# Kernel optimization log

Hardware: AMD Instinct MI355X
Metric: run time of the kernel (lower is better)

## Reference

```python
import jax, jax.numpy as jnp
import numpy as np

B, S, D, C, WD, I = 8, 14, 2048, 20, 300, 1024  # batch, imgSize, imgFeatureDim, classNum, wordFeatureDim, intermediaDim


def setup_inputs() -> dict:
    key = jax.random.key(0)
    ks = jax.random.split(key, 8)
    s = 0.02
    return {
        "imgFeaturemap": jax.random.normal(ks[0], (B, S, S, D), jnp.float32),
        "wordFeatures": jax.random.normal(ks[1], (C, WD), jnp.float32),
        "W1": jax.random.normal(ks[2], (I, D), jnp.float32) * s,   # fc1, no bias
        "W2": jax.random.normal(ks[3], (I, WD), jnp.float32) * s,  # fc2, no bias
        "W3": jax.random.normal(ks[4], (I, I), jnp.float32) * s,   # fc3
        "b3": jax.random.normal(ks[5], (I,), jnp.float32) * s,
        "W4": jax.random.normal(ks[6], (1, I), jnp.float32) * s,   # fc4
        "b4": jax.random.normal(ks[7], (1,), jnp.float32) * s,
    }


def reference(imgFeaturemap, wordFeatures, W1, W2, W3, b3, W4, b4):
    b, s, _, d = imgFeaturemap.shape
    c = wordFeatures.shape[0]
    n = b * s * s  # number of spatial locations across batch

    h_img = imgFeaturemap.reshape(n, d) @ W1.T          # [N, I]
    h_word = wordFeatures @ W2.T                         # [C, I]
    # broadcasted elementwise product + tanh (original materializes via repeat)
    t = jnp.tanh(h_img[:, None, :] * h_word[None, :, :])  # [N, C, I]
    feat = t @ W3.T + b3                                  # [N, C, I]
    coef = (feat @ W4.T)[..., 0] + b4[0]                  # [N, C]
    # softmax over spatial positions per (batch, class)
    coef = jax.nn.softmax(coef.reshape(b, s * s, c), axis=1).reshape(b, s, s, c)
    # weighted feature map and class-wise pooled semantic features
    fmwc = imgFeaturemap[:, :, :, None, :] * coef[..., None]  # [B, S, S, C, D]
    semanticFeature = fmwc.sum(axis=(1, 2))                    # [B, C, D]
    return semanticFeature, fmwc, coef
```

## Files before the change

kernel.cpp:

```cpp
#include <hip/hip_runtime.h>

typedef __attribute__((ext_vector_type(4))) float float4_t;
typedef __attribute__((ext_vector_type(8))) short short8_t;
typedef __attribute__((ext_vector_type(4))) unsigned short ushort4_t;

#define B_ 8
#define S_ 14
#define P_ 196
#define N_ 1568
#define D_ 2048
#define C_ 20
#define WD_ 300
#define I_ 1024
#define PS_ 14

__device__ __forceinline__ unsigned short f2bf(float f) {
    unsigned u = __builtin_bit_cast(unsigned, f);
    u += 0x7FFFu + ((u >> 16) & 1u);
    return (unsigned short)(u >> 16);
}

__global__ __launch_bounds__(256) void cvt_prep_kernel(const float* __restrict__ img,
                                                       const float* __restrict__ W1,
                                                       unsigned short* __restrict__ Xb,
                                                       unsigned short* __restrict__ W1b,
                                                       const float* __restrict__ wf,
                                                       const float* __restrict__ W2,
                                                       const float* __restrict__ W3,
                                                       const float* __restrict__ b3,
                                                       const float* __restrict__ W4,
                                                       const float* __restrict__ b4,
                                                       float* __restrict__ hw,
                                                       float* __restrict__ we,
                                                       float* __restrict__ bias) {
    int bid = blockIdx.x, tid = threadIdx.x;
    if (bid < 5184) {
        const float* src;
        unsigned short* dst;
        int i4;
        if (bid < 3136) { i4 = bid * 256 + tid; src = img; dst = Xb; }
        else            { i4 = (bid - 3136) * 256 + tid; src = W1; dst = W1b; }
        float4_t v = ((const float4_t*)src)[i4];
        ushort4_t o;
        o.x = f2bf(v.x); o.y = f2bf(v.y); o.z = f2bf(v.z); o.w = f2bf(v.w);
        ((ushort4_t*)dst)[i4] = o;
        return;
    }
    int pb = bid - 5184;
    if (pb < 80) {
        int idx = pb * 256 + tid;
        int c = idx >> 10, i = idx & 1023;
        const float* wr  = wf + c * WD_;
        const float* w2r = W2 + i * WD_;
        float s = 0.f;
        #pragma unroll 4
        for (int k = 0; k < WD_; k++) s += wr[k] * w2r[k];
        hw[idx] = s;
    } else if (pb < 96) {
        __shared__ float red[256];
        int blk = pb - 80;
        int i0 = blk * 64;
        int q = tid >> 6, col = tid & 63;
        float s = 0.f;
        #pragma unroll 4
        for (int j = q * 256; j < q * 256 + 256; j++)
            s += W4[j] * W3[j * I_ + i0 + col];
        red[tid] = s;
        __syncthreads();
        if (tid < 64)
            we[i0 + tid] = red[tid] + red[tid + 64] + red[tid + 128] + red[tid + 192];
    } else {
        __shared__ float r[256];
        float s = 0.f;
        for (int j = tid; j < I_; j += 256) s += b3[j] * W4[j];
        r[tid] = s;
        __syncthreads();
        for (int o = 128; o > 0; o >>= 1) {
            if (tid < o) r[tid] += r[tid + o];
            __syncthreads();
        }
        if (tid == 0) bias[0] = r[0] + b4[0];
    }
}

__global__ __launch_bounds__(256) void gemm_himg_kernel(const unsigned short* __restrict__ Xb,
                                                        const unsigned short* __restrict__ W1b,
                                                        float* __restrict__ H) {
    int wave = blockIdx.x * 4 + (threadIdx.x >> 6);
    int lane = threadIdx.x & 63;
    int kjob = 0;
    if (wave >= 784) { kjob = 1; wave -= 784; }
    int mjob = wave >> 4;
    int njob = wave & 15;
    int m0 = mjob * 32, n0 = njob * 64;
    int ra = lane & 15;
    int kq = (lane >> 4) * 8;
    int kbase = kjob * 1024;

    float4_t acc[2][4] = {};
    const unsigned short* xa = Xb  + (size_t)(m0 + ra) * D_ + kbase + kq;
    const unsigned short* wb = W1b + (size_t)(n0 + ra) * D_ + kbase + kq;

    #pragma unroll 2
    for (int k0 = 0; k0 < 1024; k0 += 32) {
        short8_t a0 = *(const short8_t*)(xa + k0);
        short8_t a1 = *(const short8_t*)(xa + 16 * D_ + k0);
        short8_t b0 = *(const short8_t*)(wb + k0);
        short8_t b1 = *(const short8_t*)(wb + 16 * D_ + k0);
        short8_t b2 = *(const short8_t*)(wb + 32 * D_ + k0);
        short8_t b3v = *(const short8_t*)(wb + 48 * D_ + k0);
        acc[0][0] = __builtin_amdgcn_mfma_f32_16x16x32_bf16(a0, b0, acc[0][0], 0, 0, 0);
        acc[0][1] = __builtin_amdgcn_mfma_f32_16x16x32_bf16(a0, b1, acc[0][1], 0, 0, 0);
        acc[0][2] = __builtin_amdgcn_mfma_f32_16x16x32_bf16(a0, b2, acc[0][2], 0, 0, 0);
        acc[0][3] = __builtin_amdgcn_mfma_f32_16x16x32_bf16(a0, b3v, acc[0][3], 0, 0, 0);
        acc[1][0] = __builtin_amdgcn_mfma_f32_16x16x32_bf16(a1, b0, acc[1][0], 0, 0, 0);
        acc[1][1] = __builtin_amdgcn_mfma_f32_16x16x32_bf16(a1, b1, acc[1][1], 0, 0, 0);
        acc[1][2] = __builtin_amdgcn_mfma_f32_16x16x32_bf16(a1, b2, acc[1][2], 0, 0, 0);
        acc[1][3] = __builtin_amdgcn_mfma_f32_16x16x32_bf16(a1, b3v, acc[1][3], 0, 0, 0);
    }

    int col = lane & 15, rq = (lane >> 4) * 4;
    float* Hk = H + (size_t)kjob * N_ * I_;
    #pragma unroll
    for (int mt = 0; mt < 2; mt++) {
        #pragma unroll
        for (int nt = 0; nt < 4; nt++) {
            float4_t v = acc[mt][nt];
            int rbase = m0 + mt * 16 + rq;
            int cidx = n0 + nt * 16 + col;
            Hk[(rbase + 0) * I_ + cidx] = v.x;
            Hk[(rbase + 1) * I_ + cidx] = v.y;
            Hk[(rbase + 2) * I_ + cidx] = v.z;
            Hk[(rbase + 3) * I_ + cidx] = v.w;
        }
    }
}

__global__ __launch_bounds__(256) void logits_kernel(const float* __restrict__ H,
                                                     const float* __restrict__ hw,
                                                     const float* __restrict__ we,
                                                     const float* __restrict__ bias,
                                                     float* __restrict__ lg) {
    __shared__ float sh[4][I_];
    __shared__ float sw[I_];
    int n0 = blockIdx.x * 4, tid = threadIdx.x;
    #pragma unroll
    for (int t = 0; t < 4; t++) {
        int idx = tid + 256 * t;
        sw[idx] = we[idx];
        #pragma unroll
        for (int nn = 0; nn < 4; nn++)
            sh[nn][idx] = H[(size_t)(n0 + nn) * I_ + idx]
                        + H[(size_t)(N_ + n0 + nn) * I_ + idx];
    }
    __syncthreads();
    int wv = tid >> 6, lane = tid & 63;
    float bz = bias[0];
    for (int j = 0; j < 5; j++) {
        int c = j * 4 + wv;
        const float* hwc = hw + c * I_;
        float a0 = 0.f, a1 = 0.f, a2 = 0.f, a3 = 0.f;
        #pragma unroll 2
        for (int i = lane; i < I_; i += 64) {
            float hv = hwc[i], wvv = sw[i];
            float x0 = sh[0][i] * hv;
            float x1 = sh[1][i] * hv;
            float x2 = sh[2][i] * hv;
            float x3 = sh[3][i] * hv;
            float t0 = 1.f - __fdividef(2.f, __expf(2.f * x0) + 1.f);
            float t1 = 1.f - __fdividef(2.f, __expf(2.f * x1) + 1.f);
            float t2 = 1.f - __fdividef(2.f, __expf(2.f * x2) + 1.f);
            float t3 = 1.f - __fdividef(2.f, __expf(2.f * x3) + 1.f);
            a0 += t0 * wvv; a1 += t1 * wvv; a2 += t2 * wvv; a3 += t3 * wvv;
        }
        #pragma unroll
        for (int o = 32; o > 0; o >>= 1) {
            a0 += __shfl_down(a0, o);
            a1 += __shfl_down(a1, o);
            a2 += __shfl_down(a2, o);
            a3 += __shfl_down(a3, o);
        }
        if (lane == 0) {
            lg[(n0 + 0) * C_ + c] = a0 + bz;
            lg[(n0 + 1) * C_ + c] = a1 + bz;
            lg[(n0 + 2) * C_ + c] = a2 + bz;
            lg[(n0 + 3) * C_ + c] = a3 + bz;
        }
    }
}

__global__ __launch_bounds__(256) void softmax_kernel(const float* __restrict__ lg,
                                                      float* __restrict__ coef) {
    __shared__ float r[4];
    __shared__ float bval;
    int bx = blockIdx.x;
    int b = bx / C_, c = bx % C_;
    int tid = threadIdx.x, wv = tid >> 6, lane = tid & 63;
    float v = (tid < P_) ? lg[(b * P_ + tid) * C_ + c] : -3.0e38f;
    float m = v;
    #pragma unroll
    for (int o = 32; o > 0; o >>= 1) m = fmaxf(m, __shfl_down(m, o));
    if (lane == 0) r[wv] = m;
    __syncthreads();
    if (tid == 0) bval = fmaxf(fmaxf(r[0], r[1]), fmaxf(r[2], r[3]));
    __syncthreads();
    float mx = bval;
    float e = (tid < P_) ? __expf(v - mx) : 0.f;
    float s = e;
    #pragma unroll
    for (int o = 32; o > 0; o >>= 1) s += __shfl_down(s, o);
    __syncthreads();
    if (lane == 0) r[wv] = s;
    __syncthreads();
    if (tid == 0) bval = r[0] + r[1] + r[2] + r[3];
    __syncthreads();
    if (tid < P_) coef[(b * P_ + tid) * C_ + c] = e / bval;
}

__global__ __launch_bounds__(256) void fmwc_kernel(const float* __restrict__ img,
                                                   const float* __restrict__ coef,
                                                   float* __restrict__ fm) {
    __shared__ float sc[C_];
    int bp = blockIdx.x, tid = threadIdx.x;
    if (tid < C_) sc[tid] = coef[bp * C_ + tid];
    __syncthreads();
    const float4_t* ir = (const float4_t*)(img + (size_t)bp * D_);
    float4_t v0 = ir[tid], v1 = ir[tid + 256];
    float4_t* ob = (float4_t*)(fm + (size_t)bp * C_ * D_);
    #pragma unroll
    for (int c = 0; c < C_; c++) {
        float s = sc[c];
        ob[c * 512 + tid] = v0 * s;
        ob[c * 512 + tid + 256] = v1 * s;
    }
}

__global__ __launch_bounds__(256) void semantic_part_kernel(const float* __restrict__ img,
                                                            const float* __restrict__ coef,
                                                            float* __restrict__ part) {
    __shared__ float sc[PS_ * C_];
    int bx = blockIdx.x;
    int ps = bx >> 4;
    int b = (bx >> 1) & 7;
    int ch = bx & 1;
    int tid = threadIdx.x;
    for (int q = tid; q < PS_ * C_; q += 256)
        sc[q] = coef[(b * P_ + ps * PS_) * C_ + q];
    __syncthreads();
    const float4_t* base = (const float4_t*)(img + (size_t)(b * P_ + ps * PS_) * D_ + ch * 1024) + tid;
    float4_t acc[C_];
    #pragma unroll
    for (int c = 0; c < C_; c++) acc[c] = (float4_t){0.f, 0.f, 0.f, 0.f};
    for (int pp = 0; pp < PS_; pp++) {
        float4_t v = base[pp * 512];
        #pragma unroll
        for (int c = 0; c < C_; c++) acc[c] += v * sc[pp * C_ + c];
    }
    float* pb = part + ((size_t)(ps * B_ + b) * C_) * D_ + ch * 1024 + tid * 4;
    #pragma unroll
    for (int c = 0; c < C_; c++) *(float4_t*)(pb + c * D_) = acc[c];
}

__global__ __launch_bounds__(256) void semantic_reduce_kernel(const float* __restrict__ part,
                                                              float* __restrict__ sem) {
    int idx = blockIdx.x * 256 + threadIdx.x;
    const float4_t* p4 = (const float4_t*)part;
    float4_t s = {0.f, 0.f, 0.f, 0.f};
    #pragma unroll
    for (int ps = 0; ps < PS_; ps++) s += p4[(size_t)ps * 81920 + idx];
    ((float4_t*)sem)[idx] = s;
}

extern "C" void kernel_launch(void* const* d_in, const int* in_sizes, int n_in,
                              void* d_out, int out_size, void* d_ws, size_t ws_size,
                              hipStream_t stream) {
    const float* img = (const float*)d_in[0];
    const float* wf  = (const float*)d_in[1];
    const float* W1  = (const float*)d_in[2];
    const float* W2  = (const float*)d_in[3];
    const float* W3  = (const float*)d_in[4];
    const float* b3  = (const float*)d_in[5];
    const float* W4  = (const float*)d_in[6];
    const float* b4  = (const float*)d_in[7];

    float* out  = (float*)d_out;
    float* sem  = out;
    float* fm   = out + (size_t)B_ * C_ * D_;
    float* coef = fm + (size_t)N_ * C_ * D_;

    char* ws = (char*)d_ws;
    unsigned short* Xb  = (unsigned short*)ws;
    unsigned short* W1b = (unsigned short*)(ws + 6422528);
    float* H    = (float*)(ws + 10616832);
    float* hw   = (float*)(ws + 23461888);
    float* we   = (float*)(ws + 23543808);
    float* bias = (float*)(ws + 23547904);
    float* lg   = (float*)(ws + 23548160);
    float* part = (float*)(ws + 23673600);

    cvt_prep_kernel<<<5281, 256, 0, stream>>>(img, W1, Xb, W1b, wf, W2, W3, b3, W4, b4, hw, we, bias);
    gemm_himg_kernel<<<392, 256, 0, stream>>>(Xb, W1b, H);
    logits_kernel<<<N_ / 4, 256, 0, stream>>>(H, hw, we, bias, lg);
    softmax_kernel<<<B_ * C_, 256, 0, stream>>>(lg, coef);
    semantic_part_kernel<<<PS_ * B_ * 2, 256, 0, stream>>>(img, coef, part);
    semantic_reduce_kernel<<<320, 256, 0, stream>>>(part, sem);
    fmwc_kernel<<<N_, 256, 0, stream>>>(img, coef, fm);
}
```

Baseline: 427.6 us.

## Fuse image GEMM with logits computation, keeping H tile in shared memory

Merges the bf16 MFMA projection GEMM and the tanh/logit reduction into one kernel. Each 1024-thread block computes a 16-row tile of H, with two K-halves summed in LDS, then computes logits for those rows directly. This removes writing and rereading the full H intermediate and one launch, at the cost of far fewer blocks (98) and repeated reads of W1 per tile.

```diff
diff --git a/kernel.cpp b/kernel.cpp
--- a/kernel.cpp
+++ b/kernel.cpp
@@ -13,6 +13,7 @@
 #define WD_ 300
 #define I_ 1024
 #define PS_ 14
+#define HLD 1025
 
 __device__ __forceinline__ unsigned short f2bf(float f) {
     unsigned u = __builtin_bit_cast(unsigned, f);
@@ -83,109 +84,72 @@
     }
 }
 
-__global__ __launch_bounds__(256) void gemm_himg_kernel(const unsigned short* __restrict__ Xb,
-                                                        const unsigned short* __restrict__ W1b,
-                                                        float* __restrict__ H) {
-    int wave = blockIdx.x * 4 + (threadIdx.x >> 6);
-    int lane = threadIdx.x & 63;
-    int kjob = 0;
-    if (wave >= 784) { kjob = 1; wave -= 784; }
-    int mjob = wave >> 4;
-    int njob = wave & 15;
-    int m0 = mjob * 32, n0 = njob * 64;
-    int ra = lane & 15;
-    int kq = (lane >> 4) * 8;
+__global__ __launch_bounds__(1024) void gemm_logits_kernel(const unsigned short* __restrict__ Xb,
+                                                           const unsigned short* __restrict__ W1b,
+                                                           const float* __restrict__ hw,
+                                                           const float* __restrict__ we,
+                                                           const float* __restrict__ bias,
+                                                           float* __restrict__ lg) {
+    __shared__ float hsh[16 * HLD];
+    __shared__ float sw[I_];
+    int tid = threadIdx.x;
+    int wave = tid >> 6, lane = tid & 63;
+    int kjob = wave >> 3, nsl = wave & 7;
+    int n0 = nsl * 128;
+    int m0 = blockIdx.x * 16;
+    int ra = lane & 15, kq = (lane >> 4) * 8;
     int kbase = kjob * 1024;
-
-    float4_t acc[2][4] = {};
+    sw[tid] = we[tid];
+
     const unsigned short* xa = Xb  + (size_t)(m0 + ra) * D_ + kbase + kq;
     const unsigned short* wb = W1b + (size_t)(n0 + ra) * D_ + kbase + kq;
 
+    float4_t acc[8] = {};
     #pragma unroll 2
     for (int k0 = 0; k0 < 1024; k0 += 32) {
-        short8_t a0 = *(const short8_t*)(xa + k0);
-        short8_t a1 = *(const short8_t*)(xa + 16 * D_ + k0);
-        short8_t b0 = *(const short8_t*)(wb + k0);
-        short8_t b1 = *(const short8_t*)(wb + 16 * D_ + k0);
-        short8_t b2 = *(const short8_t*)(wb + 32 * D_ + k0);
-        short8_t b3v = *(const short8_t*)(wb + 48 * D_ + k0);
-        acc[0][0] = __builtin_amdgcn_mfma_f32_16x16x32_bf16(a0, b0, acc[0][0], 0, 0, 0);
-        acc[0][1] = __builtin_amdgcn_mfma_f32_16x16x32_bf16(a0, b1, acc[0][1], 0, 0, 0);
-        acc[0][2] = __builtin_amdgcn_mfma_f32_16x16x32_bf16(a0, b2, acc[0][2], 0, 0, 0);
-        acc[0][3] = __builtin_amdgcn_mfma_f32_16x16x32_bf16(a0, b3v, acc[0][3], 0, 0, 0);
-        acc[1][0] = __builtin_amdgcn_mfma_f32_16x16x32_bf16(a1, b0, acc[1][0], 0, 0, 0);
-        acc[1][1] = __builtin_amdgcn_mfma_f32_16x16x32_bf16(a1, b1, acc[1][1], 0, 0, 0);
-        acc[1][2] = __builtin_amdgcn_mfma_f32_16x16x32_bf16(a1, b2, acc[1][2], 0, 0, 0);
-        acc[1][3] = __builtin_amdgcn_mfma_f32_16x16x32_bf16(a1, b3v, acc[1][3], 0, 0, 0);
-    }
-
-    int col = lane & 15, rq = (lane >> 4) * 4;
-    float* Hk = H + (size_t)kjob * N_ * I_;
-    #pragma unroll
-    for (int mt = 0; mt < 2; mt++) {
-        #pragma unroll
-        for (int nt = 0; nt < 4; nt++) {
-            float4_t v = acc[mt][nt];
-            int rbase = m0 + mt * 16 + rq;
-            int cidx = n0 + nt * 16 + col;
-            Hk[(rbase + 0) * I_ + cidx] = v.x;
-            Hk[(rbase + 1) * I_ + cidx] = v.y;
-            Hk[(rbase + 2) * I_ + cidx] = v.z;
-            Hk[(rbase + 3) * I_ + cidx] = v.w;
-        }
-    }
-}
-
-__global__ __launch_bounds__(256) void logits_kernel(const float* __restrict__ H,
-                                                     const float* __restrict__ hw,
-                                                     const float* __restrict__ we,
-                                                     const float* __restrict__ bias,
-                                                     float* __restrict__ lg) {
-    __shared__ float sh[4][I_];
-    __shared__ float sw[I_];
-    int n0 = blockIdx.x * 4, tid = threadIdx.x;
-    #pragma unroll
-    for (int t = 0; t < 4; t++) {
-        int idx = tid + 256 * t;
-        sw[idx] = we[idx];
-        #pragma unroll
-        for (int nn = 0; nn < 4; nn++)
-            sh[nn][idx] = H[(size_t)(n0 + nn) * I_ + idx]
-                        + H[(size_t)(N_ + n0 + nn) * I_ + idx];
-    }
-    __syncthreads();
-    int wv = tid >> 6, lane = tid & 63;
+        short8_t a = *(const short8_t*)(xa + k0);
+        #pragma unroll
+        for (int f = 0; f < 8; f++) {
+            short8_t b = *(const short8_t*)(wb + f * 16 * D_ + k0);
+            acc[f] = __builtin_amdgcn_mfma_f32_16x16x32_bf16(a, b, acc[f], 0, 0, 0);
+        }
+    }
+
+    int col16 = lane & 15, rq = (lane >> 4) * 4;
+    if (kjob == 0) {
+        #pragma unroll
+        for (int f = 0; f < 8; f++) {
+            float4_t v = acc[f];
+            float* hp = &hsh[rq * HLD + n0 + f * 16 + col16];
+            hp[0] = v.x; hp[HLD] = v.y; hp[2 * HLD] = v.z; hp[3 * HLD] = v.w;
+        }
+    }
+    __syncthreads();
+    if (kjob == 1) {
+        #pragma unroll
+        for (int f = 0; f < 8; f++) {
+            float4_t v = acc[f];
+            float* hp = &hsh[rq * HLD + n0 + f * 16 + col16];
+            hp[0] += v.x; hp[HLD] += v.y; hp[2 * HLD] += v.z; hp[3 * HLD] += v.w;
+        }
+    }
+    __syncthreads();
+
+    int r = wave;
     float bz = bias[0];
-    for (int j = 0; j < 5; j++) {
-        int c = j * 4 + wv;
+    const float* hr = &hsh[r * HLD];
+    for (int c = 0; c < C_; c++) {
         const float* hwc = hw + c * I_;
-        float a0 = 0.f, a1 = 0.f, a2 = 0.f, a3 = 0.f;
-        #pragma unroll 2
+        float a0 = 0.f;
+        #pragma unroll 4
         for (int i = lane; i < I_; i += 64) {
-            float hv = hwc[i], wvv = sw[i];
-            float x0 = sh[0][i] * hv;
-            float x1 = sh[1][i] * hv;
-            float x2 = sh[2][i] * hv;
-            float x3 = sh[3][i] * hv;
-            float t0 = 1.f - __fdividef(2.f, __expf(2.f * x0) + 1.f);
-            float t1 = 1.f - __fdividef(2.f, __expf(2.f * x1) + 1.f);
-            float t2 = 1.f - __fdividef(2.f, __expf(2.f * x2) + 1.f);
-            float t3 = 1.f - __fdividef(2.f, __expf(2.f * x3) + 1.f);
-            a0 += t0 * wvv; a1 += t1 * wvv; a2 += t2 * wvv; a3 += t3 * wvv;
-        }
-        #pragma unroll
-        for (int o = 32; o > 0; o >>= 1) {
-            a0 += __shfl_down(a0, o);
-            a1 += __shfl_down(a1, o);
-            a2 += __shfl_down(a2, o);
-            a3 += __shfl_down(a3, o);
-        }
-        if (lane == 0) {
-            lg[(n0 + 0) * C_ + c] = a0 + bz;
-            lg[(n0 + 1) * C_ + c] = a1 + bz;
-            lg[(n0 + 2) * C_ + c] = a2 + bz;
-            lg[(n0 + 3) * C_ + c] = a3 + bz;
-        }
+            float x = hr[i] * hwc[i];
+            float t = 1.f - __fdividef(2.f, __expf(2.f * x) + 1.f);
+            a0 += t * sw[i];
+        }
+        #pragma unroll
+        for (int o = 32; o > 0; o >>= 1) a0 += __shfl_down(a0, o);
+        if (lane == 0) lg[(m0 + r) * C_ + c] = a0 + bz;
     }
 }
 
@@ -291,16 +255,14 @@
     char* ws = (char*)d_ws;
     unsigned short* Xb  = (unsigned short*)ws;
     unsigned short* W1b = (unsigned short*)(ws + 6422528);
-    float* H    = (float*)(ws + 10616832);
-    float* hw   = (float*)(ws + 23461888);
-    float* we   = (float*)(ws + 23543808);
-    float* bias = (float*)(ws + 23547904);
-    float* lg   = (float*)(ws + 23548160);
-    float* part = (float*)(ws + 23673600);
+    float* hw   = (float*)(ws + 10616832);
+    float* we   = (float*)(ws + 10698752);
+    float* bias = (float*)(ws + 10702848);
+    float* lg   = (float*)(ws + 10703104);
+    float* part = (float*)(ws + 10828544);
 
     cvt_prep_kernel<<<5281, 256, 0, stream>>>(img, W1, Xb, W1b, wf, W2, W3, b3, W4, b4, hw, we, bias);
-    gemm_himg_kernel<<<392, 256, 0, stream>>>(Xb, W1b, H);
-    logits_kernel<<<N_ / 4, 256, 0, stream>>>(H, hw, we, bias, lg);
+    gemm_logits_kernel<<<98, 1024, 0, stream>>>(Xb, W1b, hw, we, bias, lg);
     softmax_kernel<<<B_ * C_, 256, 0, stream>>>(lg, coef);
     semantic_part_kernel<<<PS_ * B_ * 2, 256, 0, stream>>>(img, coef, part);
     semantic_reduce_kernel<<<320, 256, 0, stream>>>(part, sem);
```

After: 531.7 us. 1.24x slower.

## Stage GEMM tiles through LDS and drop split-K partial outputs

Applied to the files above, without the earlier changes.

The h_img GEMM now loads 32x64 A and 128x64 B tiles into padded shared memory and shares them across four waves, with a register prefetch of the next K slice. Each block now covers the full K=2048 range instead of splitting K across two jobs. This removes the second H partial buffer and the extra read-and-add in the logits kernel. The trade-off is two barriers per K step and fewer independent waves (392 blocks each looping 32 steps) in place of the split-K parallelism.

```diff
diff --git a/kernel.cpp b/kernel.cpp
--- a/kernel.cpp
+++ b/kernel.cpp
@@ -13,6 +13,7 @@
 #define WD_ 300
 #define I_ 1024
 #define PS_ 14
+#define LROW 72
 
 __device__ __forceinline__ unsigned short f2bf(float f) {
     unsigned u = __builtin_bit_cast(unsigned, f);
@@ -86,52 +87,79 @@
 __global__ __launch_bounds__(256) void gemm_himg_kernel(const unsigned short* __restrict__ Xb,
                                                         const unsigned short* __restrict__ W1b,
                                                         float* __restrict__ H) {
-    int wave = blockIdx.x * 4 + (threadIdx.x >> 6);
-    int lane = threadIdx.x & 63;
-    int kjob = 0;
-    if (wave >= 784) { kjob = 1; wave -= 784; }
-    int mjob = wave >> 4;
-    int njob = wave & 15;
-    int m0 = mjob * 32, n0 = njob * 64;
-    int ra = lane & 15;
-    int kq = (lane >> 4) * 8;
-    int kbase = kjob * 1024;
-
-    float4_t acc[2][4] = {};
-    const unsigned short* xa = Xb  + (size_t)(m0 + ra) * D_ + kbase + kq;
-    const unsigned short* wb = W1b + (size_t)(n0 + ra) * D_ + kbase + kq;
-
-    #pragma unroll 2
-    for (int k0 = 0; k0 < 1024; k0 += 32) {
-        short8_t a0 = *(const short8_t*)(xa + k0);
-        short8_t a1 = *(const short8_t*)(xa + 16 * D_ + k0);
-        short8_t b0 = *(const short8_t*)(wb + k0);
-        short8_t b1 = *(const short8_t*)(wb + 16 * D_ + k0);
-        short8_t b2 = *(const short8_t*)(wb + 32 * D_ + k0);
-        short8_t b3v = *(const short8_t*)(wb + 48 * D_ + k0);
-        acc[0][0] = __builtin_amdgcn_mfma_f32_16x16x32_bf16(a0, b0, acc[0][0], 0, 0, 0);
-        acc[0][1] = __builtin_amdgcn_mfma_f32_16x16x32_bf16(a0, b1, acc[0][1], 0, 0, 0);
-        acc[0][2] = __builtin_amdgcn_mfma_f32_16x16x32_bf16(a0, b2, acc[0][2], 0, 0, 0);
-        acc[0][3] = __builtin_amdgcn_mfma_f32_16x16x32_bf16(a0, b3v, acc[0][3], 0, 0, 0);
-        acc[1][0] = __builtin_amdgcn_mfma_f32_16x16x32_bf16(a1, b0, acc[1][0], 0, 0, 0);
-        acc[1][1] = __builtin_amdgcn_mfma_f32_16x16x32_bf16(a1, b1, acc[1][1], 0, 0, 0);
-        acc[1][2] = __builtin_amdgcn_mfma_f32_16x16x32_bf16(a1, b2, acc[1][2], 0, 0, 0);
-        acc[1][3] = __builtin_amdgcn_mfma_f32_16x16x32_bf16(a1, b3v, acc[1][3], 0, 0, 0);
+    __shared__ unsigned short lds[160 * LROW];
+    int tid = threadIdx.x;
+    int wave = tid >> 6, lane = tid & 63;
+    int m0 = (blockIdx.x >> 3) * 32;
+    int n0 = (blockIdx.x & 7) * 128;
+
+    int arow = tid >> 3, ak16 = tid & 7;
+    const unsigned short* gA = Xb + (size_t)(m0 + arow) * D_ + ak16 * 8;
+    unsigned short* lA = &lds[arow * LROW + ak16 * 8];
+    const unsigned short* gB[4];
+    unsigned short* lB[4];
+    #pragma unroll
+    for (int j = 0; j < 4; j++) {
+        int idx = tid + 256 * j;
+        int brow = idx >> 3, bk16 = idx & 7;
+        gB[j] = W1b + (size_t)(n0 + brow) * D_ + bk16 * 8;
+        lB[j] = &lds[(32 + brow) * LROW + bk16 * 8];
+    }
+
+    int ra = lane & 15, kq = (lane >> 4) * 8;
+    const unsigned short* Af = &lds[ra * LROW + kq];
+    const unsigned short* Bf = &lds[(32 + wave * 32 + ra) * LROW + kq];
+
+    float4_t acc[2][2] = {};
+    short8_t sA = *(const short8_t*)(gA);
+    short8_t sB0 = *(const short8_t*)(gB[0]);
+    short8_t sB1 = *(const short8_t*)(gB[1]);
+    short8_t sB2 = *(const short8_t*)(gB[2]);
+    short8_t sB3 = *(const short8_t*)(gB[3]);
+
+    for (int t = 0; t < 32; t++) {
+        *(short8_t*)lA = sA;
+        *(short8_t*)lB[0] = sB0;
+        *(short8_t*)lB[1] = sB1;
+        *(short8_t*)lB[2] = sB2;
+        *(short8_t*)lB[3] = sB3;
+        __syncthreads();
+
+        if (t < 31) {
+            int ko = (t + 1) * 64;
+            sA  = *(const short8_t*)(gA + ko);
+            sB0 = *(const short8_t*)(gB[0] + ko);
+            sB1 = *(const short8_t*)(gB[1] + ko);
+            sB2 = *(const short8_t*)(gB[2] + ko);
+            sB3 = *(const short8_t*)(gB[3] + ko);
+        }
+
+        #pragma unroll
+        for (int ks = 0; ks < 2; ks++) {
+            short8_t a0 = *(const short8_t*)(Af + ks * 32);
+            short8_t a1 = *(const short8_t*)(Af + 16 * LROW + ks * 32);
+            short8_t b0 = *(const short8_t*)(Bf + ks * 32);
+            short8_t b1 = *(const short8_t*)(Bf + 16 * LROW + ks * 32);
+            acc[0][0] = __builtin_amdgcn_mfma_f32_16x16x32_bf16(a0, b0, acc[0][0], 0, 0, 0);
+            acc[0][1] = __builtin_amdgcn_mfma_f32_16x16x32_bf16(a0, b1, acc[0][1], 0, 0, 0);
+            acc[1][0] = __builtin_amdgcn_mfma_f32_16x16x32_bf16(a1, b0, acc[1][0], 0, 0, 0);
+            acc[1][1] = __builtin_amdgcn_mfma_f32_16x16x32_bf16(a1, b1, acc[1][1], 0, 0, 0);
+        }
+        __syncthreads();
     }
 
     int col = lane & 15, rq = (lane >> 4) * 4;
-    float* Hk = H + (size_t)kjob * N_ * I_;
     #pragma unroll
     for (int mt = 0; mt < 2; mt++) {
         #pragma unroll
-        for (int nt = 0; nt < 4; nt++) {
+        for (int nt = 0; nt < 2; nt++) {
             float4_t v = acc[mt][nt];
             int rbase = m0 + mt * 16 + rq;
-            int cidx = n0 + nt * 16 + col;
-            Hk[(rbase + 0) * I_ + cidx] = v.x;
-            Hk[(rbase + 1) * I_ + cidx] = v.y;
-            Hk[(rbase + 2) * I_ + cidx] = v.z;
-            Hk[(rbase + 3) * I_ + cidx] = v.w;
+            int cidx = n0 + wave * 32 + nt * 16 + col;
+            H[(rbase + 0) * I_ + cidx] = v.x;
+            H[(rbase + 1) * I_ + cidx] = v.y;
+            H[(rbase + 2) * I_ + cidx] = v.z;
+            H[(rbase + 3) * I_ + cidx] = v.w;
         }
     }
 }
@@ -150,8 +178,7 @@
         sw[idx] = we[idx];
         #pragma unroll
         for (int nn = 0; nn < 4; nn++)
-            sh[nn][idx] = H[(size_t)(n0 + nn) * I_ + idx]
-                        + H[(size_t)(N_ + n0 + nn) * I_ + idx];
+            sh[nn][idx] = H[(size_t)(n0 + nn) * I_ + idx];
     }
     __syncthreads();
     int wv = tid >> 6, lane = tid & 63;
@@ -292,11 +319,11 @@
     unsigned short* Xb  = (unsigned short*)ws;
     unsigned short* W1b = (unsigned short*)(ws + 6422528);
     float* H    = (float*)(ws + 10616832);
-    float* hw   = (float*)(ws + 23461888);
-    float* we   = (float*)(ws + 23543808);
-    float* bias = (float*)(ws + 23547904);
-    float* lg   = (float*)(ws + 23548160);
-    float* part = (float*)(ws + 23673600);
+    float* hw   = (float*)(ws + 17039360);
+    float* we   = (float*)(ws + 17121280);
+    float* bias = (float*)(ws + 17125376);
+    float* lg   = (float*)(ws + 17125632);
+    float* part = (float*)(ws + 17251072);
 
     cvt_prep_kernel<<<5281, 256, 0, stream>>>(img, W1, Xb, W1b, wf, W2, W3, b3, W4, b4, hw, we, bias);
     gemm_himg_kernel<<<392, 256, 0, stream>>>(Xb, W1b, H);
```

Measured after the change: 403.5 us. 5.6% less time.
